# Kernel optimization log

Measured on AMD Instinct MI355X. Metric: run time of the kernel, lower is better.

Reference implementation:

```python
import jax, jax.numpy as jnp
import numpy as np
from jax import lax

MU = 3.986004418e14   # Earth GM [m^3/s^2]
A_REF = 6378136.3     # reference radius [m]


def _constants(N, dtype):
    """Precompute n1/n2 normalization tables, diagonal aBar values and the
    sub-diagonal coefficient, exactly as in compute_normalization_constants
    and the first loop of compute_aBar (these depend only on N, not on data)."""
    L = N + 2
    l = np.arange(L, dtype=np.float64)[:, None]
    m = np.arange(L, dtype=np.float64)[None, :]
    mask = l >= m + 2
    d1 = np.where(mask, (l - m) * (l + m), 1.0)
    n1 = np.where(mask, np.sqrt((2.0 * l + 1.0) * (2.0 * l - 1.0) / d1), 0.0)
    d2 = np.where(mask, (l + m) * (l - m) * (2.0 * l - 3.0), 1.0)
    num2 = np.where(mask, (l + m - 1.0) * (2.0 * l + 1.0) * (l - m - 1.0), 0.0)
    n2 = np.where(mask, np.sqrt(num2 / d2), 0.0)
    # getK(0)=1, getK(l>0)=2
    k = np.where(np.arange(L) == 0, 1.0, 2.0)
    ls = np.arange(1, L, dtype=np.float64)
    f = np.ones(L)
    f[1:] = np.sqrt((2.0 * ls + 1.0) * k[1:] / (2.0 * ls * k[:-1]))
    diag = np.cumprod(f)                  # aBar[l,l]
    sub = np.zeros(L)
    sub[1:] = np.sqrt(2.0 * ls * k[:-1] / k[1:])  # aBar[l,l-1] = sub[l]*diag[l]*u
    cast = lambda x: jnp.asarray(x, dtype=dtype)
    return cast(n1), cast(n2), cast(diag), cast(sub)


def _forward(inputs, cBar, sBar):
    N = cBar.shape[0] - 3
    L = N + 2
    dt = inputs.dtype
    r, s, t, u = inputs[:, 0], inputs[:, 1], inputs[:, 2], inputs[:, 3]
    B = r.shape[0]
    n1, n2, diag, sub = _constants(N, dt)

    # rhol[b, l] = (mu/r) * (a/r)^l  for l = 0..N  (compute_rhol)
    rho = A_REF / r
    rhol = (MU / r)[:, None] * rho[:, None] ** jnp.arange(N + 1, dtype=dt)  # [B, N+1]

    # rE[m] + i*iM[m] = (s + i t)^m, m = 0..N+1  (compute_rE_iM)
    def trig_step(c, _):
        re, im = c
        nc = (s * re - t * im, s * im + t * re)
        return nc, nc
    init = (jnp.ones_like(s), jnp.zeros_like(s))
    _, (reS, imS) = lax.scan(trig_step, init, None, length=L - 1)
    rE = jnp.concatenate([init[0][None], reS], axis=0).T  # [B, L]
    iM = jnp.concatenate([init[1][None], imS], axis=0).T  # [B, L]

    # rows of aBar for l=0 and l=1
    sqrt3 = jnp.sqrt(jnp.asarray(3.0, dt))
    row0 = jnp.zeros((B, L), dt).at[:, 0].set(1.0)
    row1 = jnp.zeros((B, L), dt).at[:, 1].set(sqrt3)
    row1 = row1.at[:, 0].set(sqrt3 * u)  # aBar[1,0] = sub[1]*diag[1]*u

    cB = cBar[:, :L].astype(dt)
    sB = sBar[:, :L].astype(dt)
    eye = jnp.eye(L, dtype=dt)

    # scan over degree l = 2..N; carry = (aBar row l-1, aBar row l-2)
    xs = (n1[2:N + 1], n2[2:N + 1], cB[2:N + 1], sB[2:N + 1],
          eye[2:N + 1], eye[1:N], diag[2:N + 1], sub[2:N + 1],
          rhol[:, 2:N + 1].T)

    def body(carry, x):
        rl1, rl2 = carry
        n1l, n2l, cl, sl, el, elm1, dl, sbl, rh = x
        # recurrence a[l,m] = u*n1[l,m]*a[l-1,m] - n2[l,m]*a[l-2,m]  (m <= l-2;
        # n1/n2 are zero elsewhere so other entries stay 0 before diag fill)
        row = u[:, None] * (n1l * rl1) - n2l * rl2
        row = row + dl * el + (sbl * dl) * u[:, None] * elm1
        contrib = rh * jnp.sum(row * (cl * rE + sl * iM), axis=1)
        return (row, rl1), contrib

    _, contribs = lax.scan(body, (row1, row0), xs)  # [N-1, B]

    pot1 = rhol[:, 1] * jnp.sum(row1 * (cB[1] * rE + sB[1] * iM), axis=1)
    potential = MU / r + pot1 + contribs.sum(axis=0)
    return (-potential)[:, None]


def setup_inputs() -> dict:
    key = jax.random.key(0)
    B, N = 65536, 64
    k1, k2, k3, k4 = jax.random.split(key, 4)
    d = jax.random.normal(k1, (B, 3), dtype=jnp.float32)
    d = d / jnp.linalg.norm(d, axis=1, keepdims=True)  # (s,t,u) direction cosines
    r = A_REF * (1.0 + jax.random.uniform(k2, (B,), dtype=jnp.float32,
                                          minval=0.05, maxval=1.0))
    inputs = jnp.concatenate([r[:, None], d], axis=1)  # [B,4] = (r,s,t,u)
    cBar = jax.random.normal(k3, (N + 3, N + 3), dtype=jnp.float32) * 1e-3
    sBar = jax.random.normal(k4, (N + 3, N + 3), dtype=jnp.float32) * 1e-3
    return {"inputs": inputs, "cBar": cBar, "sBar": sBar}


def reference(inputs, cBar, sBar):
    return _forward(inputs, cBar, sBar)
```

## Files before the change

kernel.cpp:

```cpp
#include <hip/hip_runtime.h>
#include <math.h>

#define NDEG 64
#define LMAX 66
#define LDCB 67
#define NCOL 63

#define MU_F   398600441800000.0f
#define AREF_F 6378136.3f

#define NSUB 8
#define EPW  64

struct Cons4 { float4 v[4]; };

__global__ void pines_setup(const float* __restrict__ cBar,
                            const float* __restrict__ sBar,
                            float4* __restrict__ tab,
                            float4* __restrict__ headA,
                            float4* __restrict__ headB,
                            int*    __restrict__ colstart) {
    __shared__ float s_diag[LMAX], s_sub[LMAX];
    int t = threadIdx.x;
    if (t < LMAX) {
        double d = 1.0;
        for (int l = 1; l <= t; ++l) {
            double kp = (l == 1) ? 1.0 : 2.0;
            d *= sqrt((2.0 * l + 1.0) * 2.0 / (2.0 * l * kp));
        }
        s_diag[t] = (float)d;
        double kp = (t == 1) ? 1.0 : 2.0;
        s_sub[t] = (t == 0) ? 0.0f : (float)sqrt(2.0 * t * kp / 2.0);
    }
    __syncthreads();
    if (t <= NDEG) {
        int m = t;
        headA[m] = make_float4(s_diag[m], s_sub[m + 1] * s_diag[m + 1],
                               cBar[m * LDCB + m], sBar[m * LDCB + m]);
        float cb1 = (m < NDEG) ? cBar[(m + 1) * LDCB + m] : 0.0f;
        float sb1 = (m < NDEG) ? sBar[(m + 1) * LDCB + m] : 0.0f;
        headB[m] = make_float4(cb1, sb1, 0.0f, 0.0f);

        int off = 0;
        for (int mm = 0; mm < m && mm < NCOL; ++mm)
            off += ((63 - mm + 3) >> 2) << 2;
        colstart[m] = off;

        if (m < NCOL) {
            int cnt = 63 - m;
            int pad = ((cnt + 3) >> 2) << 2;
            for (int i = 0; i < pad; ++i) {
                float4 v = make_float4(0.0f, 0.0f, 0.0f, 0.0f);
                if (i < cnt) {
                    int l = m + 2 + i;
                    float d1f = (float)((l - m) * (l + m));
                    float v1  = sqrtf((float)((2 * l + 1) * (2 * l - 1)) / d1f);
                    float d2f = (float)((l + m) * (l - m) * (2 * l - 3));
                    float n2f = (float)((l + m - 1) * (2 * l + 1) * (l - m - 1));
                    float v2  = sqrtf(n2f / d2f);
                    v = make_float4(v1, v2, cBar[l * LDCB + m], sBar[l * LDCB + m]);
                }
                tab[off + i] = v;
            }
        }
    }
}

__global__ __launch_bounds__(512) void pines_kernel(
        const float4* __restrict__ inputs,
        const float4* __restrict__ tab,
        const float4* __restrict__ headA,
        const float4* __restrict__ headB,
        const int*    __restrict__ colstart,
        float* __restrict__ out, int B) {
    __shared__ float part[NSUB][EPW];

    int t = threadIdx.x;
    int j = __builtin_amdgcn_readfirstlane(t >> 6);
    int e = t & (EPW - 1);
    int elem = blockIdx.x * EPW + e;
    int lelem = elem < B ? elem : (B - 1);

    float4 in = inputs[lelem];
    float r = in.x, ss = in.y, tt = in.z, u = in.w;

    float rho  = AREF_F / r;
    float rho2 = rho * rho;
    float ur   = u * rho;

    int d1 = 15 - 2 * j;
    int d2 = 1 + 2 * j;

    auto cpow = [&](int e_, float& re_, float& im_) {
        float br = ss, bi = tt;
        re_ = 1.0f; im_ = 0.0f;
        int ee = e_;
        while (ee) {
            if (ee & 1) {
                float nr = re_ * br - im_ * bi;
                im_ = re_ * bi + im_ * br;
                re_ = nr;
            }
            float sr = br * br - bi * bi;
            bi = 2.0f * br * bi;
            br = sr;
            ee >>= 1;
        }
    };
    auto rpow = [&](int e_) {
        float b = rho, acc = 1.0f;
        int ee = e_;
        while (ee) {
            if (ee & 1) acc *= b;
            b *= b;
            ee >>= 1;
        }
        return acc;
    };

    float re, im;      cpow(j, re, im);
    float s1r, s1i;    cpow(d1, s1r, s1i);
    float s2r, s2i;    cpow(d2, s2r, s2i);
    float rstep1 = rpow(d1);
    float rstep2 = rpow(d2);
    float rho_m  = rpow(j);

    float sum = (j == 0) ? 1.0f : 0.0f;

    int m = j;
    #pragma unroll 1
    for (int k = 0; k < 8; ++k) {
        int sm = __builtin_amdgcn_readfirstlane(m);
        float4 ha = headA[sm];
        float4 hb = headB[sm];
        float q0 = ha.x * rho_m;
        float sA = (sm >= 1) ? q0 * ha.z : 0.0f;
        float sB = (sm >= 1) ? q0 * ha.w : 0.0f;
        float q1 = (ha.y * u) * (rho_m * rho);
        sA = fmaf(q1, hb.x, sA);
        sB = fmaf(q1, hb.y, sB);

        int scol = __builtin_amdgcn_readfirstlane(colstart[sm]);
        int ng   = __builtin_amdgcn_readfirstlane((63 - sm + 3) >> 2);
        const Cons4* __restrict__ gp = (const Cons4*)(tab + scol);
        #pragma unroll 1
        for (int g = 0; g < ng; ++g) {
            Cons4 c = gp[g];
            #pragma unroll
            for (int q4 = 0; q4 < 4; ++q4) {
                float4 cc = c.v[q4];
                float t1 = cc.x * q1;
                float t2 = ur * t1;
                float t3 = cc.y * q0;
                float q  = fmaf(-rho2, t3, t2);
                sA = fmaf(q, cc.z, sA);
                sB = fmaf(q, cc.w, sB);
                q0 = q1;
                q1 = q;
            }
        }
        sum = fmaf(re, sA, sum);
        sum = fmaf(im, sB, sum);

        if (k & 1) {
            float nr = re * s2r - im * s2i;
            im = re * s2i + im * s2r; re = nr;
            rho_m *= rstep2; m += d2;
        } else {
            float nr = re * s1r - im * s1i;
            im = re * s1i + im * s1r; re = nr;
            rho_m *= rstep1; m += d1;
        }
    }
    if (j == 0) {
        float4 ha = headA[NDEG];
        float q0 = ha.x * rho_m;
        sum = fmaf(re * q0, ha.z, sum);
        sum = fmaf(im * q0, ha.w, sum);
    }

    part[j][e] = sum;
    __syncthreads();
    if (j == 0) {
        float tot = 0.0f;
        #pragma unroll
        for (int q = 0; q < NSUB; ++q) tot += part[q][e];
        if (elem < B) out[elem] = -(MU_F / r) * tot;
    }
}

extern "C" void kernel_launch(void* const* d_in, const int* in_sizes, int n_in,
                              void* d_out, int out_size, void* d_ws, size_t ws_size,
                              hipStream_t stream) {
    const float* inputs = (const float*)d_in[0];
    const float* cBar   = (const float*)d_in[1];
    const float* sBar   = (const float*)d_in[2];
    float* out = (float*)d_out;
    int B = in_sizes[0] / 4;

    float4* tab   = (float4*)d_ws;
    float4* headA = tab + 4032;
    float4* headB = headA + 65;
    int*    colst = (int*)(headB + 65);

    hipLaunchKernelGGL(pines_setup, dim3(1), dim3(128), 0, stream,
                       cBar, sBar, tab, headA, headB, colst);

    int blocks = (B + EPW - 1) / EPW;
    hipLaunchKernelGGL(pines_kernel, dim3(blocks), dim3(512), 0, stream,
                       (const float4*)inputs, tab, headA, headB, colst,
                       out, B);
}
```

Baseline: 106.8 us.

## Parallelize setup table build and software-prefetch coefficient groups in main loop

The setup kernel now fills the coefficient table with one thread per entry across many blocks, replacing the single thread per column that looped serially, and computes the diagonal terms without shared memory. The main kernel prefetches the next column's head data and column start one iteration ahead. It also double-buffers the per-group coefficient loads so the next group is fetched while the current one is computed. The prefetch reads one group past the end of each column, which relies on the following data being readable, and the extra registers may lower occupancy.

```diff
diff --git a/kernel.cpp b/kernel.cpp
--- a/kernel.cpp
+++ b/kernel.cpp
@@ -5,6 +5,7 @@
 #define LMAX 66
 #define LDCB 67
 #define NCOL 63
+#define TAB_F4 2112
 
 #define MU_F   398600441800000.0f
 #define AREF_F 6378136.3f
@@ -20,36 +21,43 @@
                             float4* __restrict__ headA,
                             float4* __restrict__ headB,
                             int*    __restrict__ colstart) {
-    __shared__ float s_diag[LMAX], s_sub[LMAX];
     int t = threadIdx.x;
-    if (t < LMAX) {
-        double d = 1.0;
-        for (int l = 1; l <= t; ++l) {
-            double kp = (l == 1) ? 1.0 : 2.0;
-            d *= sqrt((2.0 * l + 1.0) * 2.0 / (2.0 * l * kp));
-        }
-        s_diag[t] = (float)d;
-        double kp = (t == 1) ? 1.0 : 2.0;
-        s_sub[t] = (t == 0) ? 0.0f : (float)sqrt(2.0 * t * kp / 2.0);
-    }
-    __syncthreads();
-    if (t <= NDEG) {
-        int m = t;
-        headA[m] = make_float4(s_diag[m], s_sub[m + 1] * s_diag[m + 1],
-                               cBar[m * LDCB + m], sBar[m * LDCB + m]);
-        float cb1 = (m < NDEG) ? cBar[(m + 1) * LDCB + m] : 0.0f;
-        float sb1 = (m < NDEG) ? sBar[(m + 1) * LDCB + m] : 0.0f;
-        headB[m] = make_float4(cb1, sb1, 0.0f, 0.0f);
-
-        int off = 0;
-        for (int mm = 0; mm < m && mm < NCOL; ++mm)
-            off += ((63 - mm + 3) >> 2) << 2;
-        colstart[m] = off;
-
-        if (m < NCOL) {
+    if (blockIdx.x == 0) {
+        if (t <= NDEG) {
+            int m = t;
+            double d = 1.0;
+            for (int l = 1; l <= m; ++l) {
+                double kp = (l == 1) ? 1.0 : 2.0;
+                d *= sqrt((2.0 * l + 1.0) * 2.0 / (2.0 * l * kp));
+            }
+            double fnext;
+            {
+                int l = m + 1;
+                double kp = (l == 1) ? 1.0 : 2.0;
+                fnext = sqrt((2.0 * l + 1.0) * 2.0 / (2.0 * l * kp));
+            }
+            double diag1 = d * fnext;
+            double sub1  = sqrt((double)(m + 1) * ((m == 0) ? 1.0 : 2.0));
+            headA[m] = make_float4((float)d, (float)(sub1 * diag1),
+                                   cBar[m * LDCB + m], sBar[m * LDCB + m]);
+            float cb1 = (m < NDEG) ? cBar[(m + 1) * LDCB + m] : 0.0f;
+            float sb1 = (m < NDEG) ? sBar[(m + 1) * LDCB + m] : 0.0f;
+            headB[m] = make_float4(cb1, sb1, 0.0f, 0.0f);
+            int off = 0;
+            for (int mm = 0; mm < m && mm < NCOL; ++mm)
+                off += ((63 - mm + 3) >> 2) << 2;
+            colstart[m] = off;
+        }
+    } else {
+        int idx = (blockIdx.x - 1) * blockDim.x + t;
+        if (idx < NCOL * 64) {
+            int m = idx >> 6, i = idx & 63;
             int cnt = 63 - m;
             int pad = ((cnt + 3) >> 2) << 2;
-            for (int i = 0; i < pad; ++i) {
+            if (i < pad) {
+                int off = 0;
+                for (int mm = 0; mm < m; ++mm)
+                    off += ((63 - mm + 3) >> 2) << 2;
                 float4 v = make_float4(0.0f, 0.0f, 0.0f, 0.0f);
                 if (i < cnt) {
                     int l = m + 2 + i;
@@ -127,12 +135,24 @@
 
     float sum = (j == 0) ? 1.0f : 0.0f;
 
-    int m = j;
+    int ms[9];
+    ms[0] = j;
+    #pragma unroll
+    for (int k = 0; k < 8; ++k) ms[k + 1] = ms[k] + ((k & 1) ? d2 : d1);
+
+    int sm = __builtin_amdgcn_readfirstlane(ms[0]);
+    float4 ha = headA[sm];
+    float4 hb = headB[sm];
+    int scol  = __builtin_amdgcn_readfirstlane(colstart[sm]);
+
     #pragma unroll 1
     for (int k = 0; k < 8; ++k) {
-        int sm = __builtin_amdgcn_readfirstlane(m);
-        float4 ha = headA[sm];
-        float4 hb = headB[sm];
+        int smn = ms[k + 1] > 64 ? 64 : ms[k + 1];
+        smn = __builtin_amdgcn_readfirstlane(smn);
+        float4 ha_n = headA[smn];
+        float4 hb_n = headB[smn];
+        int scol_n  = __builtin_amdgcn_readfirstlane(colstart[smn]);
+
         float q0 = ha.x * rho_m;
         float sA = (sm >= 1) ? q0 * ha.z : 0.0f;
         float sB = (sm >= 1) ? q0 * ha.w : 0.0f;
@@ -140,15 +160,15 @@
         sA = fmaf(q1, hb.x, sA);
         sB = fmaf(q1, hb.y, sB);
 
-        int scol = __builtin_amdgcn_readfirstlane(colstart[sm]);
-        int ng   = __builtin_amdgcn_readfirstlane((63 - sm + 3) >> 2);
+        int ng = __builtin_amdgcn_readfirstlane((63 - sm + 3) >> 2);
         const Cons4* __restrict__ gp = (const Cons4*)(tab + scol);
+        Cons4 cur = gp[0];
         #pragma unroll 1
         for (int g = 0; g < ng; ++g) {
-            Cons4 c = gp[g];
+            Cons4 nxt = gp[g + 1];
             #pragma unroll
             for (int q4 = 0; q4 < 4; ++q4) {
-                float4 cc = c.v[q4];
+                float4 cc = cur.v[q4];
                 float t1 = cc.x * q1;
                 float t2 = ur * t1;
                 float t3 = cc.y * q0;
@@ -158,6 +178,7 @@
                 q0 = q1;
                 q1 = q;
             }
+            cur = nxt;
         }
         sum = fmaf(re, sA, sum);
         sum = fmaf(im, sB, sum);
@@ -165,15 +186,15 @@
         if (k & 1) {
             float nr = re * s2r - im * s2i;
             im = re * s2i + im * s2r; re = nr;
-            rho_m *= rstep2; m += d2;
+            rho_m *= rstep2;
         } else {
             float nr = re * s1r - im * s1i;
             im = re * s1i + im * s1r; re = nr;
-            rho_m *= rstep1; m += d1;
-        }
+            rho_m *= rstep1;
+        }
+        sm = smn; ha = ha_n; hb = hb_n; scol = scol_n;
     }
     if (j == 0) {
-        float4 ha = headA[NDEG];
         float q0 = ha.x * rho_m;
         sum = fmaf(re * q0, ha.z, sum);
         sum = fmaf(im * q0, ha.w, sum);
@@ -199,11 +220,11 @@
     int B = in_sizes[0] / 4;
 
     float4* tab   = (float4*)d_ws;
-    float4* headA = tab + 4032;
+    float4* headA = tab + TAB_F4;
     float4* headB = headA + 65;
     int*    colst = (int*)(headB + 65);
 
-    hipLaunchKernelGGL(pines_setup, dim3(1), dim3(128), 0, stream,
+    hipLaunchKernelGGL(pines_setup, dim3(17), dim3(256), 0, stream,
                        cBar, sBar, tab, headA, headB, colst);
 
     int blocks = (B + EPW - 1) / EPW;
```

Measured after the change: 90.34 us. -15.4%, faster.
